# Optimization experiments

Hardware: AMD Instinct MI355X
Metric: run time of the kernel (lower is better)

The kernel has to match this reference:

```python
import jax, jax.numpy as jnp
import numpy as np

EMBED = 1024
HEADS = 16
HEAD_DIM = EMBED // HEADS


def setup_inputs() -> dict:
    key = jax.random.key(0)
    ks = jax.random.split(key, 7)
    N, S = 2, 2048
    k = jax.random.normal(ks[0], (N, S, EMBED), dtype=jnp.float32)
    q = jax.random.normal(ks[1], (N, S, EMBED), dtype=jnp.float32)
    v = jax.random.normal(ks[2], (N, S, EMBED), dtype=jnp.float32)
    sc = 1.0 / np.sqrt(HEAD_DIM)
    # nn.Linear weights, applied as x @ W.T
    Wk = jax.random.normal(ks[3], (HEAD_DIM, HEAD_DIM), dtype=jnp.float32) * sc
    Wq = jax.random.normal(ks[4], (HEAD_DIM, HEAD_DIM), dtype=jnp.float32) * sc
    Wv = jax.random.normal(ks[5], (HEAD_DIM, HEAD_DIM), dtype=jnp.float32) * sc
    Wo = jax.random.normal(ks[6], (EMBED, EMBED), dtype=jnp.float32) / np.sqrt(EMBED)
    return {"k": k, "q": q, "v": v, "Wk": Wk, "Wq": Wq, "Wv": Wv, "Wo": Wo}


def reference(k, q, v, Wk, Wq, Wv, Wo):
    N, S, _ = q.shape
    # reshape to [N, S, H, D]; per-head projection weights shared across heads
    kh = jnp.einsum('nshd,ed->nshe', k.reshape(N, S, HEADS, HEAD_DIM), Wk)
    qh = jnp.einsum('nshd,ed->nshe', q.reshape(N, S, HEADS, HEAD_DIM), Wq)
    vh = jnp.einsum('nshd,ed->nshe', v.reshape(N, S, HEADS, HEAD_DIM), Wv)
    # energy: [N, H, q_len, k_len]
    energy = jnp.einsum('nqhd,nkhd->nhqk', qh, kh)
    attn = jax.nn.softmax(energy / jnp.sqrt(jnp.float32(HEAD_DIM)), axis=-1)
    out = jnp.einsum('nhqk,nkhd->nqhd', attn, vh).reshape(N, S, EMBED)
    return out @ Wo.T
```

## Files before the change

### kernel.cpp

```cpp
#include <hip/hip_runtime.h>

#define SQ   2048
#define HEADS 16
#define HD   64
#define EMB  1024

typedef __attribute__((ext_vector_type(2))) __fp16 h2;
typedef __attribute__((ext_vector_type(4))) __fp16 h4;
typedef __attribute__((ext_vector_type(8))) __fp16 h8;
typedef __attribute__((ext_vector_type(4))) float f4;
typedef unsigned short USH;
typedef unsigned int   UI;

__device__ __forceinline__ UI pkh(float a, float b) {
    h2 v = __builtin_amdgcn_cvt_pkrtz(a, b);
    return __builtin_bit_cast(UI, v);
}

__device__ __forceinline__ void glds16(const void* g, void* l) {
    __builtin_amdgcn_global_load_lds(
        (const __attribute__((address_space(1))) unsigned int*)g,
        (__attribute__((address_space(3))) unsigned int*)l, 16, 0, 0);
}

__global__ __launch_bounds__(256) void proj_fused(
    const float* __restrict__ q_in, const float* __restrict__ k_in,
    const float* __restrict__ v_in, const float* __restrict__ Wq,
    const float* __restrict__ Wk,   const float* __restrict__ Wv,
    const float* __restrict__ Wo,
    USH* __restrict__ Qh, USH* __restrict__ Kh, USH* __restrict__ Vt,
    USH* __restrict__ Wob)
{
    int t = threadIdx.x;
    if (blockIdx.y == 3) {
        int i = blockIdx.x * 256 + t;
        for (int j = 0; j < 4; ++j) {
            float4 v = ((const float4*)Wo)[i + j * 65536];
            uint2 pk; pk.x = pkh(v.x, v.y); pk.y = pkh(v.z, v.w);
            *(uint2*)(Wob + ((size_t)i + (size_t)j * 65536) * 4) = pk;
        }
        return;
    }
    const float* X = (blockIdx.y == 0) ? q_in : (blockIdx.y == 1) ? k_in : v_in;
    const float* W = (blockIdx.y == 0) ? Wq   : (blockIdx.y == 1) ? Wk   : Wv;
    float scale    = (blockIdx.y == 0) ? 0.18033688011112043f : 1.0f;

    int bx = (blockIdx.x & 7) * 32 + (blockIdx.x >> 3);

    __shared__ __align__(16) USH Xl[256][72];
    __shared__ __align__(16) USH Wl[64][72];

    const float4* Xg = (const float4*)(X + (size_t)bx * 16384);
    for (int j = 0; j < 16; ++j) {
        int f = t + j * 256;
        float4 v = Xg[f];
        int row = f >> 4; int col = (f & 15) << 2;
        uint2 pk; pk.x = pkh(v.x, v.y); pk.y = pkh(v.z, v.w);
        *(uint2*)&Xl[row][col] = pk;
    }
    const float4* Wg = (const float4*)W;
    for (int j = 0; j < 4; ++j) {
        int f = t + j * 256;
        float4 v = Wg[f];
        int row = f >> 4; int col = (f & 15) << 2;
        uint2 pk; pk.x = pkh(v.x, v.y); pk.y = pkh(v.z, v.w);
        *(uint2*)&Wl[row][col] = pk;
    }
    __syncthreads();

    int wv = t >> 6, lane = t & 63, l4 = lane & 15, quad = lane >> 4;

    h8 wf[4][2], xf[4][2];
    for (int et = 0; et < 4; ++et)
        for (int ks = 0; ks < 2; ++ks)
            wf[et][ks] = *(const h8*)&Wl[et * 16 + l4][ks * 32 + quad * 8];
    for (int rt = 0; rt < 4; ++rt)
        for (int ks = 0; ks < 2; ++ks)
            xf[rt][ks] = *(const h8*)&Xl[wv * 64 + rt * 16 + l4][ks * 32 + quad * 8];

    f4 acc[4][4];
    for (int et = 0; et < 4; ++et)
        for (int rt = 0; rt < 4; ++rt) acc[et][rt] = (f4)(0.0f);
    for (int et = 0; et < 4; ++et)
        for (int rt = 0; rt < 4; ++rt)
            for (int ks = 0; ks < 2; ++ks)
                acc[et][rt] = __builtin_amdgcn_mfma_f32_16x16x32_f16(
                    wf[et][ks], xf[rt][ks], acc[et][rt], 0, 0, 0);

    if (blockIdx.y == 2) {
        int ns0 = bx * 16 + wv * 4;
        int n = ns0 >> 11, s = ns0 & 2047;
        for (int et = 0; et < 4; ++et)
            for (int j = 0; j < 4; ++j) {
                int e = et * 16 + quad * 4 + j;
                uint2 pk;
                pk.x = pkh(acc[et][0][j], acc[et][1][j]);
                pk.y = pkh(acc[et][2][j], acc[et][3][j]);
                *(uint2*)(Vt + (((size_t)(n * HEADS + l4) * HD + e) * SQ + s)) = pk;
            }
    } else {
        USH* Out = (blockIdx.y == 0) ? Qh : Kh;
        for (int rt = 0; rt < 4; ++rt) {
            int ns = bx * 16 + wv * 4 + rt;
            int n = ns >> 11, s = ns & 2047;
            USH* ob = Out + (((size_t)(n * HEADS) + l4) * SQ + s) * HD;
            for (int et = 0; et < 4; ++et) {
                uint2 pk;
                pk.x = pkh(acc[et][rt][0] * scale, acc[et][rt][1] * scale);
                pk.y = pkh(acc[et][rt][2] * scale, acc[et][rt][3] * scale);
                *(uint2*)(ob + et * 16 + quad * 4) = pk;
            }
        }
    }
}

__device__ __forceinline__ void stage_kv(const USH* __restrict__ Kg,
                                         const USH* __restrict__ Vg,
                                         int kt, USH* Kd, USH* Vd,
                                         int w, int lane)
{
#pragma unroll
    for (int j = 0; j < 2; ++j) {
        int s = (w * 2 + j) * 64 + lane;
        int r = s >> 3, c = (s & 7) ^ (r & 7);
        glds16(Kg + kt * 4096 + r * 64 + c * 8, Kd + s * 8);
    }
#pragma unroll
    for (int j = 0; j < 2; ++j) {
        int s = (w * 2 + j) * 64 + lane;
        int r = s >> 3, c = (s & 7) ^ (r & 7);
        glds16(Vg + r * SQ + kt * 64 + c * 8, Vd + s * 8);
    }
}

__global__ __launch_bounds__(256, 3) void attn_kernel(
    const USH* __restrict__ Qh, const USH* __restrict__ Kh,
    const USH* __restrict__ Vt, USH* __restrict__ Oh)
{
    __shared__ union {
        struct { USH K[3][4096]; USH V[3][4096]; } s;
        struct { float Osum[64][68]; float Lsum[64]; } r;
    } lds;

    int t = threadIdx.x, w = t >> 6, lane = t & 63;
    int l4 = lane & 15, quad = lane >> 4;
    int b = blockIdx.x;
    int nh = b & 31;
    int q0 = (b >> 5) * 64;
    const USH* Qg = Qh + ((size_t)nh * SQ + q0) * HD;
    const USH* Kg = Kh + (size_t)nh * SQ * HD;
    const USH* Vg = Vt + (size_t)nh * HD * SQ;

    h8 bq[4][2];
#pragma unroll
    for (int qt = 0; qt < 4; ++qt)
#pragma unroll
        for (int ks = 0; ks < 2; ++ks)
            bq[qt][ks] = *(const h8*)(Qg + (size_t)(qt * 16 + l4) * HD + ks * 32 + quad * 8);

    f4 o[4][4];
#pragma unroll
    for (int dt = 0; dt < 4; ++dt)
#pragma unroll
        for (int qt = 0; qt < 4; ++qt) o[dt][qt] = (f4)(0.0f);
    float lsum[4] = {0.f, 0.f, 0.f, 0.f};

    int key = w * 16 + l4;
    int kslot0 = key * 8 + (quad ^ (key & 7));
    int kslot1 = key * 8 + ((4 + quad) ^ (key & 7));
    int dchunk = w * 2 + (quad >> 1);
    int vbyte  = (quad & 1) * 4;

    stage_kv(Kg, Vg, 0, lds.s.K[0], lds.s.V[0], w, lane);
    stage_kv(Kg, Vg, 1, lds.s.K[1], lds.s.V[1], w, lane);

    int cur = 0;
    for (int kt = 0; kt < SQ / 64; ++kt) {
        if (kt < SQ / 64 - 2) {
            asm volatile("s_waitcnt vmcnt(4)" ::: "memory");
        } else {
            asm volatile("s_waitcnt vmcnt(0)" ::: "memory");
        }
        __builtin_amdgcn_s_barrier();
        __builtin_amdgcn_sched_barrier(0);

        int nb = cur + 2; if (nb >= 3) nb -= 3;
        if (kt + 2 < SQ / 64)
            stage_kv(Kg, Vg, kt + 2, lds.s.K[nb], lds.s.V[nb], w, lane);

        h8 ak0 = *(const h8*)(lds.s.K[cur] + kslot0 * 8);
        h8 ak1 = *(const h8*)(lds.s.K[cur] + kslot1 * 8);

        h4 av[4];
#pragma unroll
        for (int dt = 0; dt < 4; ++dt) {
            int d = dt * 16 + l4;
            int vs = d * 8 + (dchunk ^ (d & 7));
            av[dt] = *(const h4*)(lds.s.V[cur] + vs * 8 + vbyte);
        }

        __builtin_amdgcn_s_setprio(1);
        h4 p[4];
#pragma unroll
        for (int qt = 0; qt < 4; ++qt) {
            f4 s0 = __builtin_amdgcn_mfma_f32_16x16x32_f16(ak0, bq[qt][0], (f4)(0.0f), 0, 0, 0);
            f4 sc = __builtin_amdgcn_mfma_f32_16x16x32_f16(ak1, bq[qt][1], s0, 0, 0, 0);
            float p0 = __builtin_amdgcn_exp2f(sc[0]);
            float p1 = __builtin_amdgcn_exp2f(sc[1]);
            float p2 = __builtin_amdgcn_exp2f(sc[2]);
            float p3 = __builtin_amdgcn_exp2f(sc[3]);
            lsum[qt] += (p0 + p1) + (p2 + p3);
            uint2 u; u.x = pkh(p0, p1); u.y = pkh(p2, p3);
            p[qt] = __builtin_bit_cast(h4, u);
        }
#pragma unroll
        for (int dt = 0; dt < 4; ++dt)
#pragma unroll
            for (int qt = 0; qt < 4; ++qt)
                o[dt][qt] = __builtin_amdgcn_mfma_f32_16x16x16f16(
                    av[dt], p[qt], o[dt][qt], 0, 0, 0);
        __builtin_amdgcn_s_setprio(0);

        cur = cur + 1 == 3 ? 0 : cur + 1;
    }

#pragma unroll
    for (int qt = 0; qt < 4; ++qt) {
        lsum[qt] += __shfl_xor(lsum[qt], 16, 64);
        lsum[qt] += __shfl_xor(lsum[qt], 32, 64);
    }

    __syncthreads();
    for (int ph = 0; ph < 4; ++ph) {
        if (w == ph) {
            for (int dt = 0; dt < 4; ++dt)
                for (int qt = 0; qt < 4; ++qt) {
                    float* dst = &lds.r.Osum[qt * 16 + l4][dt * 16 + quad * 4];
                    f4 val = o[dt][qt];
                    if (ph) val += *(const f4*)dst;
                    *(f4*)dst = val;
                }
            if (quad == 0)
                for (int qt = 0; qt < 4; ++qt) {
                    int qi = qt * 16 + l4;
                    lds.r.Lsum[qi] = ph ? (lds.r.Lsum[qi] + lsum[qt]) : lsum[qt];
                }
        }
        __syncthreads();
    }

    int n = nh >> 4, h = nh & 15;
    int q = t >> 2, d0 = (t & 3) * 16;
    float inv = 1.0f / lds.r.Lsum[q];
    float vv[16];
#pragma unroll
    for (int i = 0; i < 4; ++i) {
        f4 x = *(const f4*)&lds.r.Osum[q][d0 + i * 4];
        vv[i * 4 + 0] = x[0] * inv; vv[i * 4 + 1] = x[1] * inv;
        vv[i * 4 + 2] = x[2] * inv; vv[i * 4 + 3] = x[3] * inv;
    }
    uint4 ou0, ou1;
    ou0.x = pkh(vv[0], vv[1]);   ou0.y = pkh(vv[2], vv[3]);
    ou0.z = pkh(vv[4], vv[5]);   ou0.w = pkh(vv[6], vv[7]);
    ou1.x = pkh(vv[8], vv[9]);   ou1.y = pkh(vv[10], vv[11]);
    ou1.z = pkh(vv[12], vv[13]); ou1.w = pkh(vv[14], vv[15]);
    USH* ob = Oh + ((size_t)(n * SQ + q0 + q)) * EMB + h * HD + d0;
    *(uint4*)ob = ou0;
    *(uint4*)(ob + 8) = ou1;
}

__global__ __launch_bounds__(256, 4) void gemm_bt(const USH* __restrict__ A,
                                                  const USH* __restrict__ B,
                                                  float* __restrict__ C)
{
    __shared__ __align__(16) USH Al[2][4096];
    __shared__ __align__(16) USH Bl[2][4096];
    int t = threadIdx.x, w = t >> 6, lane = t & 63;
    int l4 = lane & 15, quad = lane >> 4;
    int b = blockIdx.x;
    int m0 = (b & 63) * 64;
    int n0 = (b >> 6) * 64;
    int wm = (w >> 1) * 32, wn = (w & 1) * 32;

    f4 acc[2][2];
    for (int mt = 0; mt < 2; ++mt)
        for (int nt = 0; nt < 2; ++nt) acc[mt][nt] = (f4)(0.0f);

    int aslot[2][2], bslot[2][2];
#pragma unroll
    for (int mt = 0; mt < 2; ++mt)
#pragma unroll
        for (int ks = 0; ks < 2; ++ks) {
            int m = wm + mt * 16 + l4;
            aslot[mt][ks] = m * 8 + ((ks * 4 + quad) ^ (m & 7));
            int nn = wn + mt * 16 + l4;
            bslot[mt][ks] = nn * 8 + ((ks * 4 + quad) ^ (nn & 7));
        }

#pragma unroll
    for (int j = 0; j < 2; ++j) {
        int s = (w * 2 + j) * 64 + lane;
        int r = s >> 3, c = (s & 7) ^ (r & 7);
        glds16(A + (size_t)(m0 + r) * 1024 + c * 8, Al[0] + s * 8);
        glds16(B + (size_t)(n0 + r) * 1024 + c * 8, Bl[0] + s * 8);
    }

    for (int ki = 0; ki < 16; ++ki) {
        int cur = ki & 1;
        __syncthreads();
        if (ki + 1 < 16) {
            int k0 = (ki + 1) * 64;
#pragma unroll
            for (int j = 0; j < 2; ++j) {
                int s = (w * 2 + j) * 64 + lane;
                int r = s >> 3, c = (s & 7) ^ (r & 7);
                glds16(A + (size_t)(m0 + r) * 1024 + k0 + c * 8, Al[cur ^ 1] + s * 8);
                glds16(B + (size_t)(n0 + r) * 1024 + k0 + c * 8, Bl[cur ^ 1] + s * 8);
            }
        }

        h8 a[2][2], bf[2][2];
#pragma unroll
        for (int mt = 0; mt < 2; ++mt)
#pragma unroll
            for (int ks = 0; ks < 2; ++ks) {
                a[mt][ks]  = *(const h8*)(Al[cur] + aslot[mt][ks] * 8);
                bf[mt][ks] = *(const h8*)(Bl[cur] + bslot[mt][ks] * 8);
            }
#pragma unroll
        for (int mt = 0; mt < 2; ++mt)
#pragma unroll
            for (int nt = 0; nt < 2; ++nt)
#pragma unroll
                for (int ks = 0; ks < 2; ++ks)
                    acc[mt][nt] = __builtin_amdgcn_mfma_f32_16x16x32_f16(
                        a[mt][ks], bf[nt][ks], acc[mt][nt], 0, 0, 0);
    }

    for (int mt = 0; mt < 2; ++mt)
        for (int nt = 0; nt < 2; ++nt)
            for (int r = 0; r < 4; ++r)
                C[(size_t)(m0 + wm + mt * 16 + quad * 4 + r) * 1024 +
                  (n0 + wn + nt * 16 + l4)] = acc[mt][nt][r];
}

extern "C" void kernel_launch(void* const* d_in, const int* in_sizes, int n_in,
                              void* d_out, int out_size, void* d_ws, size_t ws_size,
                              hipStream_t stream) {
    const float* k_in = (const float*)d_in[0];
    const float* q_in = (const float*)d_in[1];
    const float* v_in = (const float*)d_in[2];
    const float* Wk   = (const float*)d_in[3];
    const float* Wq   = (const float*)d_in[4];
    const float* Wv   = (const float*)d_in[5];
    const float* Wo   = (const float*)d_in[6];
    float* out = (float*)d_out;

    char* ws = (char*)d_ws;
    USH* Qh  = (USH*)(ws);
    USH* Kh  = (USH*)(ws + 8388608);
    USH* Vt  = (USH*)(ws + 16777216);
    USH* Oh  = (USH*)(ws + 25165824);
    USH* Wob = (USH*)(ws + 33554432);

    proj_fused<<<dim3(256, 4), dim3(256), 0, stream>>>(
        q_in, k_in, v_in, Wq, Wk, Wv, Wo, Qh, Kh, Vt, Wob);
    attn_kernel<<<dim3(1024), dim3(256), 0, stream>>>(Qh, Kh, Vt, Oh);
    gemm_bt<<<dim3(1024), dim3(256), 0, stream>>>(Oh, Wob, out);
}
```

Before: 193.6 us.

## Process two key tiles per iteration and use 16x16x32 MFMA for PV

The attention loop now handles two 64-key tiles per iteration. The P·V product uses the wider 16x16x32 f16 MFMA, whose K=32 operand is built by concatenating the P and V fragments of both tiles, halving the number of PV MFMA instructions. The K buffer is double-buffered and the V buffer ring has four slots. The explicit vmcnt-based triple-buffer pipeline is replaced by two __syncthreads per pair of tiles, and the s_setprio hints are removed. This may expose load latency, since prefetch is only one tile ahead and each sync waits for all outstanding loads.

```diff
diff --git a/kernel.cpp b/kernel.cpp
--- a/kernel.cpp
+++ b/kernel.cpp
@@ -114,10 +114,8 @@
     }
 }
 
-__device__ __forceinline__ void stage_kv(const USH* __restrict__ Kg,
-                                         const USH* __restrict__ Vg,
-                                         int kt, USH* Kd, USH* Vd,
-                                         int w, int lane)
+__device__ __forceinline__ void stage_k(const USH* __restrict__ Kg,
+                                        int kt, USH* Kd, int w, int lane)
 {
 #pragma unroll
     for (int j = 0; j < 2; ++j) {
@@ -125,6 +123,10 @@
         int r = s >> 3, c = (s & 7) ^ (r & 7);
         glds16(Kg + kt * 4096 + r * 64 + c * 8, Kd + s * 8);
     }
+}
+__device__ __forceinline__ void stage_v(const USH* __restrict__ Vg,
+                                        int kt, USH* Vd, int w, int lane)
+{
 #pragma unroll
     for (int j = 0; j < 2; ++j) {
         int s = (w * 2 + j) * 64 + lane;
@@ -138,7 +140,7 @@
     const USH* __restrict__ Vt, USH* __restrict__ Oh)
 {
     __shared__ union {
-        struct { USH K[3][4096]; USH V[3][4096]; } s;
+        struct { USH K[2][4096]; USH V[4][4096]; } s;
         struct { float Osum[64][68]; float Lsum[64]; } r;
     } lds;
 
@@ -170,58 +172,84 @@
     int kslot1 = key * 8 + ((4 + quad) ^ (key & 7));
     int dchunk = w * 2 + (quad >> 1);
     int vbyte  = (quad & 1) * 4;
-
-    stage_kv(Kg, Vg, 0, lds.s.K[0], lds.s.V[0], w, lane);
-    stage_kv(Kg, Vg, 1, lds.s.K[1], lds.s.V[1], w, lane);
-
-    int cur = 0;
-    for (int kt = 0; kt < SQ / 64; ++kt) {
-        if (kt < SQ / 64 - 2) {
-            asm volatile("s_waitcnt vmcnt(4)" ::: "memory");
-        } else {
-            asm volatile("s_waitcnt vmcnt(0)" ::: "memory");
-        }
-        __builtin_amdgcn_s_barrier();
-        __builtin_amdgcn_sched_barrier(0);
-
-        int nb = cur + 2; if (nb >= 3) nb -= 3;
-        if (kt + 2 < SQ / 64)
-            stage_kv(Kg, Vg, kt + 2, lds.s.K[nb], lds.s.V[nb], w, lane);
-
-        h8 ak0 = *(const h8*)(lds.s.K[cur] + kslot0 * 8);
-        h8 ak1 = *(const h8*)(lds.s.K[cur] + kslot1 * 8);
-
-        h4 av[4];
+    int vs[4];
+#pragma unroll
+    for (int dt = 0; dt < 4; ++dt) {
+        int d = dt * 16 + l4;
+        vs[dt] = (d * 8 + (dchunk ^ (d & 7))) * 8 + vbyte;
+    }
+
+    stage_k(Kg, 0, lds.s.K[0], w, lane);
+    stage_v(Vg, 0, lds.s.V[0], w, lane);
+
+    uint2 pA[4];
+    for (int i = 0; i < 16; ++i) {
+        int t0 = 2 * i, t1 = 2 * i + 1;
+        USH* Vb0 = lds.s.V[t0 & 3];
+        USH* Vb1 = lds.s.V[t1 & 3];
+
+        __syncthreads();
+        stage_k(Kg, t0 + 1, lds.s.K[1], w, lane);
+        stage_v(Vg, t0 + 1, Vb1, w, lane);
+
+        {
+            h8 ak0 = *(const h8*)(lds.s.K[0] + kslot0 * 8);
+            h8 ak1 = *(const h8*)(lds.s.K[0] + kslot1 * 8);
+#pragma unroll
+            for (int qt = 0; qt < 4; ++qt) {
+                f4 s0 = __builtin_amdgcn_mfma_f32_16x16x32_f16(ak0, bq[qt][0], (f4)(0.0f), 0, 0, 0);
+                f4 sc = __builtin_amdgcn_mfma_f32_16x16x32_f16(ak1, bq[qt][1], s0, 0, 0, 0);
+                float p0 = __builtin_amdgcn_exp2f(sc[0]);
+                float p1 = __builtin_amdgcn_exp2f(sc[1]);
+                float p2 = __builtin_amdgcn_exp2f(sc[2]);
+                float p3 = __builtin_amdgcn_exp2f(sc[3]);
+                lsum[qt] += (p0 + p1) + (p2 + p3);
+                pA[qt].x = pkh(p0, p1); pA[qt].y = pkh(p2, p3);
+            }
+        }
+
+        __syncthreads();
+        if (t1 + 1 < 32) {
+            stage_k(Kg, t1 + 1, lds.s.K[0], w, lane);
+            stage_v(Vg, t1 + 1, lds.s.V[(t1 + 1) & 3], w, lane);
+        }
+
+        uint2 pB[4];
+        {
+            h8 ak0 = *(const h8*)(lds.s.K[1] + kslot0 * 8);
+            h8 ak1 = *(const h8*)(lds.s.K[1] + kslot1 * 8);
+#pragma unroll
+            for (int qt = 0; qt < 4; ++qt) {
+                f4 s0 = __builtin_amdgcn_mfma_f32_16x16x32_f16(ak0, bq[qt][0], (f4)(0.0f), 0, 0, 0);
+                f4 sc = __builtin_amdgcn_mfma_f32_16x16x32_f16(ak1, bq[qt][1], s0, 0, 0, 0);
+                float p0 = __builtin_amdgcn_exp2f(sc[0]);
+                float p1 = __builtin_amdgcn_exp2f(sc[1]);
+                float p2 = __builtin_amdgcn_exp2f(sc[2]);
+                float p3 = __builtin_amdgcn_exp2f(sc[3]);
+                lsum[qt] += (p0 + p1) + (p2 + p3);
+                pB[qt].x = pkh(p0, p1); pB[qt].y = pkh(p2, p3);
+            }
+        }
+
+        h8 av8[4];
 #pragma unroll
         for (int dt = 0; dt < 4; ++dt) {
-            int d = dt * 16 + l4;
-            int vs = d * 8 + (dchunk ^ (d & 7));
-            av[dt] = *(const h4*)(lds.s.V[cur] + vs * 8 + vbyte);
-        }
-
-        __builtin_amdgcn_s_setprio(1);
-        h4 p[4];
-#pragma unroll
-        for (int qt = 0; qt < 4; ++qt) {
-            f4 s0 = __builtin_amdgcn_mfma_f32_16x16x32_f16(ak0, bq[qt][0], (f4)(0.0f), 0, 0, 0);
-            f4 sc = __builtin_amdgcn_mfma_f32_16x16x32_f16(ak1, bq[qt][1], s0, 0, 0, 0);
-            float p0 = __builtin_amdgcn_exp2f(sc[0]);
-            float p1 = __builtin_amdgcn_exp2f(sc[1]);
-            float p2 = __builtin_amdgcn_exp2f(sc[2]);
-            float p3 = __builtin_amdgcn_exp2f(sc[3]);
-            lsum[qt] += (p0 + p1) + (p2 + p3);
-            uint2 u; u.x = pkh(p0, p1); u.y = pkh(p2, p3);
-            p[qt] = __builtin_bit_cast(h4, u);
-        }
+            uint2 lo = *(const uint2*)(Vb0 + vs[dt]);
+            uint2 hi = *(const uint2*)(Vb1 + vs[dt]);
+            uint4 u; u.x = lo.x; u.y = lo.y; u.z = hi.x; u.w = hi.y;
+            av8[dt] = __builtin_bit_cast(h8, u);
+        }
+
 #pragma unroll
         for (int dt = 0; dt < 4; ++dt)
 #pragma unroll
-            for (int qt = 0; qt < 4; ++qt)
-                o[dt][qt] = __builtin_amdgcn_mfma_f32_16x16x16f16(
-                    av[dt], p[qt], o[dt][qt], 0, 0, 0);
-        __builtin_amdgcn_s_setprio(0);
-
-        cur = cur + 1 == 3 ? 0 : cur + 1;
+            for (int qt = 0; qt < 4; ++qt) {
+                uint4 u; u.x = pA[qt].x; u.y = pA[qt].y;
+                u.z = pB[qt].x; u.w = pB[qt].y;
+                h8 pp = __builtin_bit_cast(h8, u);
+                o[dt][qt] = __builtin_amdgcn_mfma_f32_16x16x32_f16(
+                    av8[dt], pp, o[dt][qt], 0, 0, 0);
+            }
     }
 
 #pragma unroll
```

Result: faster. 187.0 us (-3.4%).

## Use per-wave private LDS stripes to drop block barriers and fuse PV into 16x16x32 MFMA

Applied to the files above, without the earlier changes.

Each wave now stages only its own 16-key stripe of K and V into a private triple-buffered LDS region. Because no wave reads another wave's stripe, the per-tile block barrier is removed and each wave synchronises only on its own vmcnt. Two key tiles are processed per iteration so that the PV product can use the 16x16x32 MFMA with concatenated probability vectors, halving the PV MFMA count. The cost is a full vmcnt(0) drain per iteration, which shortens the effective prefetch depth, and the setprio hints are dropped.

```diff
diff --git a/kernel.cpp b/kernel.cpp
--- a/kernel.cpp
+++ b/kernel.cpp
@@ -114,22 +114,22 @@
     }
 }
 
-__device__ __forceinline__ void stage_kv(const USH* __restrict__ Kg,
-                                         const USH* __restrict__ Vg,
-                                         int kt, USH* Kd, USH* Vd,
-                                         int w, int lane)
+__device__ __forceinline__ void stage_stripe(const USH* __restrict__ Kg,
+                                             const USH* __restrict__ Vg,
+                                             int kt, USH* wbuf,
+                                             int w, int lane)
 {
 #pragma unroll
     for (int j = 0; j < 2; ++j) {
-        int s = (w * 2 + j) * 64 + lane;
-        int r = s >> 3, c = (s & 7) ^ (r & 7);
-        glds16(Kg + kt * 4096 + r * 64 + c * 8, Kd + s * 8);
+        int chunk = (lane >> 4) + j * 4;
+        glds16(Kg + (size_t)(kt * 64 + w * 16 + (lane & 15)) * HD + chunk * 8,
+               wbuf + j * 512);
     }
 #pragma unroll
     for (int j = 0; j < 2; ++j) {
-        int s = (w * 2 + j) * 64 + lane;
-        int r = s >> 3, c = (s & 7) ^ (r & 7);
-        glds16(Vg + r * SQ + kt * 64 + c * 8, Vd + s * 8);
+        int d = ((lane >> 5) + j * 2) * 16 + ((lane & 31) >> 1);
+        glds16(Vg + (size_t)d * SQ + kt * 64 + w * 16 + (lane & 1) * 8,
+               wbuf + 1024 + j * 512);
     }
 }
 
@@ -138,7 +138,7 @@
     const USH* __restrict__ Vt, USH* __restrict__ Oh)
 {
     __shared__ union {
-        struct { USH K[3][4096]; USH V[3][4096]; } s;
+        USH wbuf[4][3][2048];
         struct { float Osum[64][68]; float Lsum[64]; } r;
     } lds;
 
@@ -165,63 +165,70 @@
         for (int qt = 0; qt < 4; ++qt) o[dt][qt] = (f4)(0.0f);
     float lsum[4] = {0.f, 0.f, 0.f, 0.f};
 
-    int key = w * 16 + l4;
-    int kslot0 = key * 8 + (quad ^ (key & 7));
-    int kslot1 = key * 8 + ((4 + quad) ^ (key & 7));
-    int dchunk = w * 2 + (quad >> 1);
-    int vbyte  = (quad & 1) * 4;
-
-    stage_kv(Kg, Vg, 0, lds.s.K[0], lds.s.V[0], w, lane);
-    stage_kv(Kg, Vg, 1, lds.s.K[1], lds.s.V[1], w, lane);
-
-    int cur = 0;
-    for (int kt = 0; kt < SQ / 64; ++kt) {
-        if (kt < SQ / 64 - 2) {
-            asm volatile("s_waitcnt vmcnt(4)" ::: "memory");
-        } else {
-            asm volatile("s_waitcnt vmcnt(0)" ::: "memory");
-        }
-        __builtin_amdgcn_s_barrier();
+    int koff = quad * 128 + l4 * 8;
+    int voff = 1024 + l4 * 16 + quad * 4;
+
+    stage_stripe(Kg, Vg, 0, lds.wbuf[w][0], w, lane);
+    stage_stripe(Kg, Vg, 1, lds.wbuf[w][1], w, lane);
+
+    for (int i = 0; i < 16; ++i) {
+        int tA = 2 * i, tB = 2 * i + 1;
+        USH* bufA = lds.wbuf[w][tA % 3];
+        USH* bufB = lds.wbuf[w][tB % 3];
+
+        asm volatile("s_waitcnt vmcnt(0)" ::: "memory");
         __builtin_amdgcn_sched_barrier(0);
 
-        int nb = cur + 2; if (nb >= 3) nb -= 3;
-        if (kt + 2 < SQ / 64)
-            stage_kv(Kg, Vg, kt + 2, lds.s.K[nb], lds.s.V[nb], w, lane);
-
-        h8 ak0 = *(const h8*)(lds.s.K[cur] + kslot0 * 8);
-        h8 ak1 = *(const h8*)(lds.s.K[cur] + kslot1 * 8);
-
-        h4 av[4];
+        h8 akA0 = *(const h8*)(bufA + koff);
+        h8 akA1 = *(const h8*)(bufA + 512 + koff);
+        h8 akB0 = *(const h8*)(bufB + koff);
+        h8 akB1 = *(const h8*)(bufB + 512 + koff);
+        h8 av8[4];
 #pragma unroll
         for (int dt = 0; dt < 4; ++dt) {
-            int d = dt * 16 + l4;
-            int vs = d * 8 + (dchunk ^ (d & 7));
-            av[dt] = *(const h4*)(lds.s.V[cur] + vs * 8 + vbyte);
-        }
-
-        __builtin_amdgcn_s_setprio(1);
-        h4 p[4];
+            uint2 lo = *(const uint2*)(bufA + voff + dt * 256);
+            uint2 hi = *(const uint2*)(bufB + voff + dt * 256);
+            uint4 u; u.x = lo.x; u.y = lo.y; u.z = hi.x; u.w = hi.y;
+            av8[dt] = __builtin_bit_cast(h8, u);
+        }
+        asm volatile("s_waitcnt lgkmcnt(0)" ::: "memory");
+        __builtin_amdgcn_sched_barrier(0);
+        if (i < 15) {
+            stage_stripe(Kg, Vg, tA + 2, lds.wbuf[w][(tA + 2) % 3], w, lane);
+            stage_stripe(Kg, Vg, tB + 2, lds.wbuf[w][(tB + 2) % 3], w, lane);
+        }
+
+        uint2 pA[4];
 #pragma unroll
         for (int qt = 0; qt < 4; ++qt) {
-            f4 s0 = __builtin_amdgcn_mfma_f32_16x16x32_f16(ak0, bq[qt][0], (f4)(0.0f), 0, 0, 0);
-            f4 sc = __builtin_amdgcn_mfma_f32_16x16x32_f16(ak1, bq[qt][1], s0, 0, 0, 0);
+            f4 s0 = __builtin_amdgcn_mfma_f32_16x16x32_f16(akA0, bq[qt][0], (f4)(0.0f), 0, 0, 0);
+            f4 sc = __builtin_amdgcn_mfma_f32_16x16x32_f16(akA1, bq[qt][1], s0, 0, 0, 0);
             float p0 = __builtin_amdgcn_exp2f(sc[0]);
             float p1 = __builtin_amdgcn_exp2f(sc[1]);
             float p2 = __builtin_amdgcn_exp2f(sc[2]);
             float p3 = __builtin_amdgcn_exp2f(sc[3]);
             lsum[qt] += (p0 + p1) + (p2 + p3);
-            uint2 u; u.x = pkh(p0, p1); u.y = pkh(p2, p3);
-            p[qt] = __builtin_bit_cast(h4, u);
-        }
-#pragma unroll
-        for (int dt = 0; dt < 4; ++dt)
-#pragma unroll
-            for (int qt = 0; qt < 4; ++qt)
-                o[dt][qt] = __builtin_amdgcn_mfma_f32_16x16x16f16(
-                    av[dt], p[qt], o[dt][qt], 0, 0, 0);
-        __builtin_amdgcn_s_setprio(0);
-
-        cur = cur + 1 == 3 ? 0 : cur + 1;
+            pA[qt].x = pkh(p0, p1); pA[qt].y = pkh(p2, p3);
+        }
+
+#pragma unroll
+        for (int qt = 0; qt < 4; ++qt) {
+            f4 s0 = __builtin_amdgcn_mfma_f32_16x16x32_f16(akB0, bq[qt][0], (f4)(0.0f), 0, 0, 0);
+            f4 sc = __builtin_amdgcn_mfma_f32_16x16x32_f16(akB1, bq[qt][1], s0, 0, 0, 0);
+            float p0 = __builtin_amdgcn_exp2f(sc[0]);
+            float p1 = __builtin_amdgcn_exp2f(sc[1]);
+            float p2 = __builtin_amdgcn_exp2f(sc[2]);
+            float p3 = __builtin_amdgcn_exp2f(sc[3]);
+            lsum[qt] += (p0 + p1) + (p2 + p3);
+            uint4 u;
+            u.x = pA[qt].x; u.y = pA[qt].y;
+            u.z = pkh(p0, p1); u.w = pkh(p2, p3);
+            h8 pp = __builtin_bit_cast(h8, u);
+#pragma unroll
+            for (int dt = 0; dt < 4; ++dt)
+                o[dt][qt] = __builtin_amdgcn_mfma_f32_16x16x32_f16(
+                    av8[dt], pp, o[dt][qt], 0, 0, 0);
+        }
     }
 
 #pragma unroll
```

Result: faster. 182.5 us (-5.8%).
